# Kernel tuning notes

Hardware: AMD Instinct MI355X
Metric: run time of the kernel (lower is better)

## Reference

```python
import jax, jax.numpy as jnp
import numpy as np
from jax import lax

V, E, Q, D = 100000, 300, 64, 4096
K = 5
NEG_SLOPE = 0.01


def setup_inputs() -> dict:
    key = jax.random.key(0)
    ks = jax.random.split(key, 16)
    return {
        "question": jax.random.randint(ks[0], (Q,), 0, V),
        "doc1": jax.random.randint(ks[1], (D,), 0, V),
        "doc2": jax.random.randint(ks[2], (D,), 0, V),
        "doc1_sim": jax.random.uniform(ks[3], (D, Q), dtype=jnp.float32),
        "doc2_sim": jax.random.uniform(ks[4], (D, Q), dtype=jnp.float32),
        "gaf": jax.random.normal(ks[5], (4,), dtype=jnp.float32),
        "baf": jax.random.normal(ks[6], (4,), dtype=jnp.float32),
        "emb": jax.random.normal(ks[7], (V, E), dtype=jnp.float32) * 0.1,
        "idf": jax.random.uniform(ks[8], (V, 1), dtype=jnp.float32) * 10.0,
        "conv_w": jax.random.normal(ks[9], (E, E, 3), dtype=jnp.float32) * (1.0 / np.sqrt(3 * E)),
        "conv_b": jax.random.normal(ks[10], (E,), dtype=jnp.float32) * 0.01,
        "qw_w": jax.random.normal(ks[11], (1, E + 1), dtype=jnp.float32) * (1.0 / np.sqrt(E + 1)),
        "qw_b": jax.random.normal(ks[12], (1,), dtype=jnp.float32) * 0.01,
        "lin1_w": jax.random.normal(ks[13], (8, 6), dtype=jnp.float32) * (1.0 / np.sqrt(6)),
        "lin2_w": jax.random.normal(ks[14], (1, 8), dtype=jnp.float32) * (1.0 / np.sqrt(8)),
        "out_w": jax.random.normal(ks[15], (1, 5), dtype=jnp.float32) * (1.0 / np.sqrt(5)),
    }


def _leaky(x):
    return jnp.where(x >= 0, x, NEG_SLOPE * x)


def _conv_residual(x, w, b):
    # x: [L, E]. Torch Conv1d(E,E,3,padding=2) followed by slice [1:L+1] is a
    # centered SAME conv; activation applied before the residual add.
    y = lax.conv_general_dilated(x.T[None], w, (1,), [(1, 1)],
                                 dimension_numbers=("NCW", "OIW", "NCW"))
    y = y[0] + b[:, None]            # [E, L]
    return _leaky(y).T + x           # [L, E]


def _cosine(A, B):
    # A: [Q, E], B: [L, E] -> [Q, L]
    num = A @ B.T
    den = jnp.linalg.norm(A, axis=-1)[:, None] * jnp.linalg.norm(B, axis=-1)[None, :]
    return num / den


def _kmax_pool(sim):
    # sim: [Q, L] -> [Q, 2] = (max, mean of top-K)
    top = lax.top_k(sim, K)[0]       # descending [Q, K]
    return jnp.stack([top[:, 0], jnp.mean(top, axis=-1)], axis=-1)


def _get_output(pooled_list, q_weights, lin1_w, lin2_w):
    temp = jnp.concatenate(pooled_list, axis=-1)     # [Q, 6]
    lo = _leaky(temp @ lin1_w.T) @ lin2_w.T          # [Q, 1]
    lo = lo[:, 0] * q_weights
    return jnp.sum(lo) / lo.shape[0]


def reference(question, doc1, doc2, doc1_sim, doc2_sim, gaf, baf,
              emb, idf, conv_w, conv_b, qw_w, qw_b, lin1_w, lin2_w, out_w):
    q_emb = emb[question]            # [Q, E]
    d1_emb = emb[doc1]               # [D, E]
    d2_emb = emb[doc2]

    sim_ins_d1 = _cosine(q_emb, d1_emb)
    sim_ins_d2 = _cosine(q_emb, d2_emb)

    q_conv = _conv_residual(q_emb, conv_w, conv_b)
    d1_conv = _conv_residual(d1_emb, conv_w, conv_b)
    d2_conv = _conv_residual(d2_emb, conv_w, conv_b)

    sim_sen_d1 = _cosine(q_conv, d1_conv)
    sim_sen_d2 = _cosine(q_conv, d2_conv)

    sim_oh_d1 = doc1_sim.T           # [Q, D]
    sim_oh_d2 = doc2_sim.T

    p_oh_d1, p_ins_d1, p_sen_d1 = _kmax_pool(sim_oh_d1), _kmax_pool(sim_ins_d1), _kmax_pool(sim_sen_d1)
    p_oh_d2, p_ins_d2, p_sen_d2 = _kmax_pool(sim_oh_d2), _kmax_pool(sim_ins_d2), _kmax_pool(sim_sen_d2)

    q_idfs = idf[question]           # [Q, 1]
    qw = jnp.concatenate([q_conv, q_idfs], axis=-1) @ qw_w.T + qw_b  # [Q, 1]
    q_weights = jax.nn.softmax(qw[:, 0], axis=-1)

    doc1_emit = _get_output([p_oh_d1, p_ins_d1, p_sen_d1], q_weights, lin1_w, lin2_w)
    doc2_emit = _get_output([p_oh_d2, p_ins_d2, p_sen_d2], q_weights, lin1_w, lin2_w)

    good_feats = jnp.concatenate([gaf, doc1_emit[None]])  # [5]
    bad_feats = jnp.concatenate([baf, doc2_emit[None]])
    good_out = out_w @ good_feats                          # [1]
    bad_out = out_w @ bad_feats

    loss1 = jnp.mean(jnp.maximum(0.0, -(good_out - bad_out) + 1.0))
    return (loss1, good_out, bad_out, loss1, loss1)
```

## Files before the change

### kernel.cpp

```cpp
#include <hip/hip_runtime.h>
#include <math.h>

#define EE 300
#define KP 320
#define LDSW 328
#define QQ 64
#define DD 4096
#define NEG 0.01f

typedef __attribute__((ext_vector_type(8))) short short8;
typedef __attribute__((ext_vector_type(4))) float f32x4;
typedef unsigned short ushort_t;

__device__ inline ushort_t f2bf(float f) {
  unsigned u = __builtin_bit_cast(unsigned, f);
  u += 0x7fff + ((u >> 16) & 1);
  return (ushort_t)(u >> 16);
}
__device__ inline float bf2f(ushort_t h) {
  return __builtin_bit_cast(float, (unsigned)h << 16);
}
__device__ inline void top5_insert(float* t, float v) {
  if (v > t[4]) {
    t[4] = v;
    #pragma unroll
    for (int j = 4; j > 0; --j)
      if (t[j] > t[j - 1]) { float tmp = t[j]; t[j] = t[j - 1]; t[j - 1] = tmp; }
  }
}

#define GATHER_ROWS (66 + 4098 + 4098)
#define GATHER_BLOCKS ((GATHER_ROWS + 3) / 4)
#define WT_BLOCKS 143
#define ZERO_BLOCKS 9
#define OHPOOL_BLOCKS 256
#define PREP_BLOCKS (GATHER_BLOCKS + WT_BLOCKS + ZERO_BLOCKS + OHPOOL_BLOCKS)

__global__ __launch_bounds__(256) void prep(
    const float* __restrict__ emb, const int* __restrict__ question,
    const int* __restrict__ doc1, const int* __restrict__ doc2,
    const float* __restrict__ conv_w,
    const float* __restrict__ doc1_sim, const float* __restrict__ doc2_sim,
    ushort_t* __restrict__ qbe, ushort_t* __restrict__ d1be, ushort_t* __restrict__ d2be,
    ushort_t* __restrict__ qbc, ushort_t* __restrict__ d1bc, ushort_t* __restrict__ d2bc,
    ushort_t* __restrict__ wt2,
    float* __restrict__ nq2, float* __restrict__ nd12, float* __restrict__ nd22,
    float* __restrict__ zero_base, float* __restrict__ pt5) {
  __shared__ float strip[64][33];
  int b = blockIdx.x;
  int tid = threadIdx.x;
  int wv = tid >> 6, lane = tid & 63;
  if (b < GATHER_BLOCKS) {
    int g = b * 4 + wv;
    if (g >= GATHER_ROWS) return;
    int t, row;
    if (g < 66)             { t = 0; row = g; }
    else if (g < 66 + 4098) { t = 1; row = g - 66; }
    else                    { t = 2; row = g - 4164; }
    const int* idx = t == 0 ? question : (t == 1 ? doc1 : doc2);
    int L = t == 0 ? QQ : DD;
    ushort_t* be = t == 0 ? qbe : (t == 1 ? d1be : d2be);
    ushort_t* bc = t == 0 ? qbc : (t == 1 ? d1bc : d2bc);
    float* nrm2 = t == 0 ? nq2 : (t == 1 ? nd12 : nd22);
    if (row == 0 || row == L + 1) {
      for (int i = lane; i < KP; i += 64) be[(size_t)row * KP + i] = 0;
      return;
    }
    int r = row - 1;
    const float* src = emb + (size_t)idx[r] * EE;
    float ss = 0.f;
    for (int i = lane; i < EE; i += 64) {
      float v = src[i];
      be[(size_t)row * KP + i] = f2bf(v);
      ss += v * v;
    }
    for (int i = EE + lane; i < KP; i += 64) {
      be[(size_t)row * KP + i] = 0;
      bc[(size_t)r * KP + i] = 0;
    }
    #pragma unroll
    for (int o = 32; o; o >>= 1) ss += __shfl_xor(ss, o);
    if (lane == 0) nrm2[r] = ss;
  } else if (b < GATHER_BLOCKS + WT_BLOCKS) {
    int f = (b - GATHER_BLOCKS) * 4 + wv;
    if (f >= 570) return;
    int ks = f % 10, n = (f / 10) % 19, tap = f / 190;
    int o = n * 16 + (lane & 15);
    int kbase = ks * 32 + (lane >> 4) * 8;
    ushort_t* dst = wt2 + (size_t)f * 512 + lane * 8;
    #pragma unroll
    for (int e = 0; e < 8; ++e) {
      int k = kbase + e;
      float v = (o < EE && k < EE) ? conv_w[((size_t)o * EE + k) * 3 + tap] : 0.f;
      dst[e] = f2bf(v);
    }
  } else if (b < GATHER_BLOCKS + WT_BLOCKS + ZERO_BLOCKS) {
    int i0 = (b - (GATHER_BLOCKS + WT_BLOCKS)) * 1024 + tid;
    #pragma unroll
    for (int j = 0; j < 4; ++j) {
      int i = i0 + j * 256;
      if (i < 8320) zero_base[i] = 0.f;
    }
  } else {
    int ob = b - (GATHER_BLOCKS + WT_BLOCKS + ZERO_BLOCKS);
    int o = ob >> 7, chunk = ob & 127;
    int ps = o ? 3 : 0;
    const float* dsim = o ? doc2_sim : doc1_sim;
    int l0 = chunk * 32;
    int r = tid >> 3, q0 = (tid & 7) * 8;
    const float* srcp = dsim + (size_t)(l0 + r) * QQ + q0;
    f32x4 v0 = *(const f32x4*)srcp;
    f32x4 v1 = *(const f32x4*)(srcp + 4);
    #pragma unroll
    for (int e = 0; e < 4; ++e) strip[q0 + e][r] = v0[e];
    #pragma unroll
    for (int e = 0; e < 4; ++e) strip[q0 + 4 + e][r] = v1[e];
    __syncthreads();
    if (tid < 64) {
      float t5[5] = {-1e30f, -1e30f, -1e30f, -1e30f, -1e30f};
      #pragma unroll
      for (int l = 0; l < 32; ++l) top5_insert(t5, strip[tid][l]);
      float* dst = pt5 + (((size_t)ps * QQ + tid) * 128 + chunk) * 8;
      *(f32x4*)dst = (f32x4){t5[0], t5[1], t5[2], t5[3]};
      *(f32x4*)(dst + 4) = (f32x4){t5[4], -1e30f, -1e30f, -1e30f};
    }
  }
}

__global__ __launch_bounds__(256) void conv_mfma(
    const ushort_t* __restrict__ wt2, const float* __restrict__ bias,
    const float* __restrict__ qw_w,
    const ushort_t* __restrict__ qbe, const ushort_t* __restrict__ d1be,
    const ushort_t* __restrict__ d2be,
    ushort_t* __restrict__ qbc, ushort_t* __restrict__ d1bc,
    ushort_t* __restrict__ d2bc,
    float* __restrict__ nqc2, float* __restrict__ nd1c2, float* __restrict__ nd2c2,
    float* __restrict__ qwacc) {
  __shared__ ushort_t lds[34 * LDSW];
  int bx = blockIdx.x;
  int t, m0, yh;
  if (bx < 4) { t = 0; m0 = (bx >> 1) * 32; yh = bx & 1; }
  else {
    int i = bx - 4;
    t = 1 + (i >> 8);
    int j = i & 255;
    m0 = (j >> 1) * 32; yh = j & 1;
  }
  const ushort_t* be = t == 0 ? qbe : (t == 1 ? d1be : d2be);
  ushort_t* bc = t == 0 ? qbc : (t == 1 ? d1bc : d2bc);
  float* nc2 = t == 0 ? nqc2 : (t == 1 ? nd1c2 : nd2c2);
  int tid = threadIdx.x;
  for (int s = tid; s < 34 * 40; s += 256) {
    int row = s / 40, col = s - row * 40;
    *(short8*)(&lds[row * LDSW + col * 8]) =
        *(const short8*)(be + (size_t)(m0 + row) * KP + col * 8);
  }
  __syncthreads();
  int wv = tid >> 6, lane = tid & 63, mrow = lane & 15, g = lane >> 4;
  int nstart, ncnt;
  if (yh == 0) { nstart = (wv < 2) ? 3 * wv : 2 * wv + 2; ncnt = (wv < 2) ? 3 : 2; }
  else         { nstart = (wv == 0) ? 10 : 2 * wv + 11;   ncnt = (wv == 0) ? 3 : 2; }
  f32x4 acc[3][2];
  #pragma unroll
  for (int j = 0; j < 3; ++j)
    #pragma unroll
    for (int h = 0; h < 2; ++h) acc[j][h] = (f32x4){0.f, 0.f, 0.f, 0.f};

  for (int tap = 0; tap < 3; ++tap) {
    const ushort_t* alo = &lds[(mrow + tap) * LDSW + g * 8];
    #pragma unroll
    for (int ks = 0; ks < 10; ++ks) {
      short8 a0 = *(const short8*)(alo + ks * 32);
      short8 a1 = *(const short8*)(alo + 16 * LDSW + ks * 32);
      #pragma unroll
      for (int j = 0; j < 3; ++j) {
        if (j < ncnt) {
          short8 bfr = *(const short8*)(wt2 +
              (size_t)((tap * 19 + nstart + j) * 10 + ks) * 512 + lane * 8);
          acc[j][0] = __builtin_amdgcn_mfma_f32_16x16x32_bf16(a0, bfr, acc[j][0], 0, 0, 0);
          acc[j][1] = __builtin_amdgcn_mfma_f32_16x16x32_bf16(a1, bfr, acc[j][1], 0, 0, 0);
        }
      }
    }
  }
  float ss[2][4] = {{0.f,0.f,0.f,0.f},{0.f,0.f,0.f,0.f}};
  float yq[2][4] = {{0.f,0.f,0.f,0.f},{0.f,0.f,0.f,0.f}};
  #pragma unroll
  for (int j = 0; j < 3; ++j) {
    if (j < ncnt) {
      int col = (nstart + j) * 16 + mrow;
      if (col < EE) {
        float bcol = bias[col];
        float qwc = (t == 0) ? qw_w[col] : 0.f;
        #pragma unroll
        for (int h = 0; h < 2; ++h) {
          #pragma unroll
          for (int r = 0; r < 4; ++r) {
            int lrow = h * 16 + g * 4 + r;
            float y = acc[j][h][r] + bcol;
            y = (y >= 0.f) ? y : NEG * y;
            y += bf2f(lds[(1 + lrow) * LDSW + col]);
            bc[(size_t)(m0 + lrow) * KP + col] = f2bf(y);
            ss[h][r] += y * y;
            if (t == 0) yq[h][r] += y * qwc;
          }
        }
      }
    }
  }
  #pragma unroll
  for (int h = 0; h < 2; ++h) {
    #pragma unroll
    for (int r = 0; r < 4; ++r) {
      float s = ss[h][r];
      s += __shfl_xor(s, 1); s += __shfl_xor(s, 2);
      s += __shfl_xor(s, 4); s += __shfl_xor(s, 8);
      if (mrow == 0) atomicAdd(&nc2[m0 + h * 16 + g * 4 + r], s);
      if (t == 0) {
        float sq = yq[h][r];
        sq += __shfl_xor(sq, 1); sq += __shfl_xor(sq, 2);
        sq += __shfl_xor(sq, 4); sq += __shfl_xor(sq, 8);
        if (mrow == 0) atomicAdd(&qwacc[m0 + h * 16 + g * 4 + r], sq);
      }
    }
  }
}

__global__ __launch_bounds__(256) void sim_pool(
    const ushort_t* __restrict__ qbe, const ushort_t* __restrict__ d1be,
    const ushort_t* __restrict__ d2be,
    const ushort_t* __restrict__ qbc, const ushort_t* __restrict__ d1bc,
    const ushort_t* __restrict__ d2bc,
    const float* __restrict__ nq2, const float* __restrict__ nd12,
    const float* __restrict__ nd22, const float* __restrict__ nqc2,
    const float* __restrict__ nd1c2, const float* __restrict__ nd2c2,
    float* __restrict__ pt5) {
  __shared__ ushort_t ldsB[32 * LDSW];
  __shared__ float strip[64][33];
  int s = blockIdx.x >> 7, chunk = blockIdx.x & 127;
  int ps = (s == 0) ? 1 : (s == 1) ? 4 : (s == 2) ? 2 : 5;
  int l0 = chunk * 32;
  const ushort_t* A = (s < 2) ? qbe + KP : qbc;
  const ushort_t* B = s == 0 ? d1be + KP : s == 1 ? d2be + KP
                    : s == 2 ? d1bc : d2bc;
  const float* na2 = (s < 2) ? nq2 : nqc2;
  const float* nb2 = s == 0 ? nd12 : s == 1 ? nd22 : s == 2 ? nd1c2 : nd2c2;
  int tid = threadIdx.x;
  for (int i = tid; i < 32 * 40; i += 256) {
    int row = i / 40, col = i - row * 40;
    *(short8*)(&ldsB[row * LDSW + col * 8]) =
        *(const short8*)(B + (size_t)(l0 + row) * KP + col * 8);
  }
  __syncthreads();
  int wv = tid >> 6, lane = tid & 63, mrow = lane & 15, g = lane >> 4;
  f32x4 acc[2];
  acc[0] = (f32x4){0.f, 0.f, 0.f, 0.f};
  acc[1] = (f32x4){0.f, 0.f, 0.f, 0.f};
  const ushort_t* arow = A + (size_t)(wv * 16 + mrow) * KP + g * 8;
  #pragma unroll
  for (int ks = 0; ks < 10; ++ks) {
    short8 a = *(const short8*)(arow + ks * 32);
    #pragma unroll
    for (int n = 0; n < 2; ++n) {
      short8 bfr = *(const short8*)(&ldsB[(n * 16 + mrow) * LDSW + g * 8 + ks * 32]);
      acc[n] = __builtin_amdgcn_mfma_f32_16x16x32_bf16(a, bfr, acc[n], 0, 0, 0);
    }
  }
  #pragma unroll
  for (int n = 0; n < 2; ++n) {
    int l = n * 16 + mrow;
    float inb = rsqrtf(nb2[l0 + l]);
    #pragma unroll
    for (int r = 0; r < 4; ++r) {
      int q = wv * 16 + g * 4 + r;
      strip[q][l] = acc[n][r] * rsqrtf(na2[q]) * inb;
    }
  }
  __syncthreads();
  if (tid < 64) {
    float t5[5] = {-1e30f, -1e30f, -1e30f, -1e30f, -1e30f};
    #pragma unroll
    for (int l = 0; l < 32; ++l) top5_insert(t5, strip[tid][l]);
    float* dst = pt5 + (((size_t)ps * QQ + tid) * 128 + chunk) * 8;
    *(f32x4*)dst = (f32x4){t5[0], t5[1], t5[2], t5[3]};
    *(f32x4*)(dst + 4) = (f32x4){t5[4], -1e30f, -1e30f, -1e30f};
  }
}

__global__ __launch_bounds__(256) void merge(
    const float* __restrict__ pt5, float* __restrict__ pool) {
  int widx = blockIdx.x * 4 + (threadIdx.x >> 6);
  int lane = threadIdx.x & 63;
  int src = widx >> 6, q = widx & 63;
  const float* p0 = pt5 + (((size_t)src * QQ + q) * 128 + 2 * lane) * 8;
  float t5[5] = {-1e30f, -1e30f, -1e30f, -1e30f, -1e30f};
  #pragma unroll
  for (int c = 0; c < 2; ++c)
    #pragma unroll
    for (int j = 0; j < 5; ++j) top5_insert(t5, p0[c * 8 + j]);
  #pragma unroll
  for (int mask = 1; mask < 64; mask <<= 1) {
    float a[5], bb[5];
    #pragma unroll
    for (int j = 0; j < 5; ++j) { a[j] = t5[j]; bb[j] = __shfl_xor(t5[j], mask); }
    int ia = 0, ib = 0;
    #pragma unroll
    for (int j = 0; j < 5; ++j) t5[j] = (a[ia] >= bb[ib]) ? a[ia++] : bb[ib++];
  }
  if (lane == 0) {
    float sm = t5[0] + t5[1] + t5[2] + t5[3] + t5[4];
    pool[((size_t)src * QQ + q) * 2 + 0] = t5[0];
    pool[((size_t)src * QQ + q) * 2 + 1] = sm * 0.2f;
  }
}

__global__ void final_kernel(
    const float* __restrict__ qwacc, const float* __restrict__ idf,
    const int* __restrict__ question, const float* __restrict__ qw_w,
    const float* __restrict__ qw_b, const float* __restrict__ pool,
    const float* __restrict__ lin1_w, const float* __restrict__ lin2_w,
    const float* __restrict__ out_w, const float* __restrict__ gaf,
    const float* __restrict__ baf, float* __restrict__ out5) {
  int q = threadIdx.x;
  float s = qwacc[q] + qw_b[0] + idf[question[q]] * qw_w[EE];
  float m = s;
  #pragma unroll
  for (int o = 32; o; o >>= 1) m = fmaxf(m, __shfl_xor(m, o));
  float e = expf(s - m);
  float se = e;
  #pragma unroll
  for (int o = 32; o; o >>= 1) se += __shfl_xor(se, o);
  float qwgt = e / se;

  float emit[2];
  for (int doc = 0; doc < 2; ++doc) {
    float temp[6];
    #pragma unroll
    for (int j = 0; j < 3; ++j) {
      temp[2 * j]     = pool[(((size_t)doc * 3 + j) * QQ + q) * 2 + 0];
      temp[2 * j + 1] = pool[(((size_t)doc * 3 + j) * QQ + q) * 2 + 1];
    }
    float lo = 0.f;
    #pragma unroll
    for (int r = 0; r < 8; ++r) {
      float h = 0.f;
      #pragma unroll
      for (int c = 0; c < 6; ++c) h += lin1_w[r * 6 + c] * temp[c];
      h = (h >= 0.f) ? h : NEG * h;
      lo += lin2_w[r] * h;
    }
    lo *= qwgt;
    #pragma unroll
    for (int o = 32; o; o >>= 1) lo += __shfl_xor(lo, o);
    emit[doc] = lo / (float)QQ;
  }
  if (q == 0) {
    float good = out_w[0] * gaf[0] + out_w[1] * gaf[1] + out_w[2] * gaf[2] +
                 out_w[3] * gaf[3] + out_w[4] * emit[0];
    float bad  = out_w[0] * baf[0] + out_w[1] * baf[1] + out_w[2] * baf[2] +
                 out_w[3] * baf[3] + out_w[4] * emit[1];
    float l1 = fmaxf(0.f, -(good - bad) + 1.f);
    out5[0] = l1; out5[1] = good; out5[2] = bad; out5[3] = l1; out5[4] = l1;
  }
}

extern "C" void kernel_launch(void* const* d_in, const int* in_sizes, int n_in,
                              void* d_out, int out_size, void* d_ws, size_t ws_size,
                              hipStream_t stream) {
  (void)in_sizes; (void)n_in; (void)out_size; (void)ws_size;
  const int* question   = (const int*)d_in[0];
  const int* doc1       = (const int*)d_in[1];
  const int* doc2       = (const int*)d_in[2];
  const float* doc1_sim = (const float*)d_in[3];
  const float* doc2_sim = (const float*)d_in[4];
  const float* gaf      = (const float*)d_in[5];
  const float* baf      = (const float*)d_in[6];
  const float* emb      = (const float*)d_in[7];
  const float* idf      = (const float*)d_in[8];
  const float* conv_w   = (const float*)d_in[9];
  const float* conv_b   = (const float*)d_in[10];
  const float* qw_w     = (const float*)d_in[11];
  const float* qw_b     = (const float*)d_in[12];
  const float* lin1_w   = (const float*)d_in[13];
  const float* lin2_w   = (const float*)d_in[14];
  const float* out_w    = (const float*)d_in[15];
  float* out = (float*)d_out;

  char* p = (char*)d_ws;
  ushort_t* qbe  = (ushort_t*)p; p += (size_t)(QQ + 2) * KP * 2;
  ushort_t* d1be = (ushort_t*)p; p += (size_t)(DD + 2) * KP * 2;
  ushort_t* d2be = (ushort_t*)p; p += (size_t)(DD + 2) * KP * 2;
  ushort_t* qbc  = (ushort_t*)p; p += (size_t)QQ * KP * 2;
  ushort_t* d1bc = (ushort_t*)p; p += (size_t)DD * KP * 2;
  ushort_t* d2bc = (ushort_t*)p; p += (size_t)DD * KP * 2;
  ushort_t* wt2  = (ushort_t*)p; p += (size_t)570 * 512 * 2;
  float* nq2   = (float*)p; p += QQ * 4;
  float* nd12  = (float*)p; p += DD * 4;
  float* nd22  = (float*)p; p += DD * 4;
  float* nqc2  = (float*)p; p += QQ * 4;
  float* nd1c2 = (float*)p; p += DD * 4;
  float* nd2c2 = (float*)p; p += DD * 4;
  float* qwacc = (float*)p; p += QQ * 4;
  float* pt5   = (float*)p; p += (size_t)6 * QQ * 128 * 8 * 4;
  float* pool  = (float*)p; p += 6 * QQ * 2 * 4;

  prep<<<PREP_BLOCKS, 256, 0, stream>>>(
      emb, question, doc1, doc2, conv_w, doc1_sim, doc2_sim,
      qbe, d1be, d2be, qbc, d1bc, d2bc, wt2,
      nq2, nd12, nd22, nqc2, pt5);

  conv_mfma<<<516, 256, 0, stream>>>(
      wt2, conv_b, qw_w, qbe, d1be, d2be, qbc, d1bc, d2bc,
      nqc2, nd1c2, nd2c2, qwacc);

  sim_pool<<<512, 256, 0, stream>>>(
      qbe, d1be, d2be, qbc, d1bc, d2bc,
      nq2, nd12, nd22, nqc2, nd1c2, nd2c2, pt5);

  merge<<<96, 256, 0, stream>>>(pt5, pool);

  final_kernel<<<1, 64, 0, stream>>>(qwacc, idf, question, qw_w, qw_b, pool,
                                     lin1_w, lin2_w, out_w, gaf, baf, out);
}
```

Before: 57.59 us.

## Fuse ins-sim into conv kernel, merge pooling into sen-sim and final kernels

The embedding-similarity top-k work now runs as extra blocks inside the conv kernel, since it only depends on the gathered embeddings. The sentence-similarity blocks run alongside the merge of the already-finished pools, and the remaining merges move into the final kernel. Chunks grow from 32 to 64 rows, and the conv tile grows from 32 to 64 rows per block. This removes two launches and halves the partial top-5 buffer. In exchange there are fewer, heavier blocks, more accumulator registers in the conv, and a serial merge loop in a single-block final kernel.

Measured after the change: 129.4 us. +124.8%, slower.

```diff
diff --git a/kernel.cpp b/kernel.cpp
--- a/kernel.cpp
+++ b/kernel.cpp
@@ -28,12 +28,74 @@
       if (t[j] > t[j - 1]) { float tmp = t[j]; t[j] = t[j - 1]; t[j - 1] = tmp; }
   }
 }
+__device__ inline void wave_merge5(float* t5) {
+  #pragma unroll
+  for (int mask = 1; mask < 64; mask <<= 1) {
+    float a[5], bb[5];
+    #pragma unroll
+    for (int j = 0; j < 5; ++j) { a[j] = t5[j]; bb[j] = __shfl_xor(t5[j], mask); }
+    int ia = 0, ib = 0;
+    #pragma unroll
+    for (int j = 0; j < 5; ++j) t5[j] = (a[ia] >= bb[ib]) ? a[ia++] : bb[ib++];
+  }
+}
+
+#define SMEM_BYTES (66 * LDSW * 2)
+
+__device__ void sim64(const ushort_t* __restrict__ A, const ushort_t* __restrict__ B,
+                      const float* __restrict__ na2, const float* __restrict__ nb2,
+                      int chunk, int ps, float* __restrict__ pt5, char* smem) {
+  ushort_t* ldsB = (ushort_t*)smem;
+  float (*strip)[65] = (float(*)[65])smem;
+  int l0 = chunk * 64;
+  int tid = threadIdx.x;
+  for (int i = tid; i < 64 * 40; i += 256) {
+    int row = i / 40, col = i - row * 40;
+    *(short8*)(&ldsB[row * LDSW + col * 8]) =
+        *(const short8*)(B + (size_t)(l0 + row) * KP + col * 8);
+  }
+  __syncthreads();
+  int wv = tid >> 6, lane = tid & 63, mrow = lane & 15, g = lane >> 4;
+  f32x4 acc[4];
+  #pragma unroll
+  for (int n = 0; n < 4; ++n) acc[n] = (f32x4){0.f, 0.f, 0.f, 0.f};
+  const ushort_t* arow = A + (size_t)(wv * 16 + mrow) * KP + g * 8;
+  #pragma unroll
+  for (int ks = 0; ks < 10; ++ks) {
+    short8 a = *(const short8*)(arow + ks * 32);
+    #pragma unroll
+    for (int n = 0; n < 4; ++n) {
+      short8 bfr = *(const short8*)(&ldsB[(n * 16 + mrow) * LDSW + g * 8 + ks * 32]);
+      acc[n] = __builtin_amdgcn_mfma_f32_16x16x32_bf16(a, bfr, acc[n], 0, 0, 0);
+    }
+  }
+  __syncthreads();
+  #pragma unroll
+  for (int n = 0; n < 4; ++n) {
+    int l = n * 16 + mrow;
+    float inb = rsqrtf(nb2[l0 + l]);
+    #pragma unroll
+    for (int r = 0; r < 4; ++r) {
+      int q = wv * 16 + g * 4 + r;
+      strip[q][l] = acc[n][r] * rsqrtf(na2[q]) * inb;
+    }
+  }
+  __syncthreads();
+  if (tid < 64) {
+    float t5[5] = {-1e30f, -1e30f, -1e30f, -1e30f, -1e30f};
+    #pragma unroll
+    for (int l = 0; l < 64; ++l) top5_insert(t5, strip[tid][l]);
+    float* dst = pt5 + (((size_t)ps * QQ + tid) * 64 + chunk) * 8;
+    *(f32x4*)dst = (f32x4){t5[0], t5[1], t5[2], t5[3]};
+    *(f32x4*)(dst + 4) = (f32x4){t5[4], -1e30f, -1e30f, -1e30f};
+  }
+}
 
 #define GATHER_ROWS (66 + 4098 + 4098)
 #define GATHER_BLOCKS ((GATHER_ROWS + 3) / 4)
 #define WT_BLOCKS 143
 #define ZERO_BLOCKS 9
-#define OHPOOL_BLOCKS 256
+#define OHPOOL_BLOCKS 128
 #define PREP_BLOCKS (GATHER_BLOCKS + WT_BLOCKS + ZERO_BLOCKS + OHPOOL_BLOCKS)
 
 __global__ __launch_bounds__(256) void prep(
@@ -46,7 +108,7 @@
     ushort_t* __restrict__ wt2,
     float* __restrict__ nq2, float* __restrict__ nd12, float* __restrict__ nd22,
     float* __restrict__ zero_base, float* __restrict__ pt5) {
-  __shared__ float strip[64][33];
+  __shared__ float strip[64][65];
   int b = blockIdx.x;
   int tid = threadIdx.x;
   int wv = tid >> 6, lane = tid & 63;
@@ -103,54 +165,64 @@
     }
   } else {
     int ob = b - (GATHER_BLOCKS + WT_BLOCKS + ZERO_BLOCKS);
-    int o = ob >> 7, chunk = ob & 127;
+    int o = ob >> 6, chunk = ob & 63;
     int ps = o ? 3 : 0;
     const float* dsim = o ? doc2_sim : doc1_sim;
-    int l0 = chunk * 32;
-    int r = tid >> 3, q0 = (tid & 7) * 8;
+    int l0 = chunk * 64;
+    int r = tid >> 2, q0 = (tid & 3) * 16;
     const float* srcp = dsim + (size_t)(l0 + r) * QQ + q0;
-    f32x4 v0 = *(const f32x4*)srcp;
-    f32x4 v1 = *(const f32x4*)(srcp + 4);
-    #pragma unroll
-    for (int e = 0; e < 4; ++e) strip[q0 + e][r] = v0[e];
-    #pragma unroll
-    for (int e = 0; e < 4; ++e) strip[q0 + 4 + e][r] = v1[e];
+    #pragma unroll
+    for (int c = 0; c < 4; ++c) {
+      f32x4 v = *(const f32x4*)(srcp + c * 4);
+      #pragma unroll
+      for (int e = 0; e < 4; ++e) strip[q0 + c * 4 + e][r] = v[e];
+    }
     __syncthreads();
     if (tid < 64) {
       float t5[5] = {-1e30f, -1e30f, -1e30f, -1e30f, -1e30f};
       #pragma unroll
-      for (int l = 0; l < 32; ++l) top5_insert(t5, strip[tid][l]);
-      float* dst = pt5 + (((size_t)ps * QQ + tid) * 128 + chunk) * 8;
+      for (int l = 0; l < 64; ++l) top5_insert(t5, strip[tid][l]);
+      float* dst = pt5 + (((size_t)ps * QQ + tid) * 64 + chunk) * 8;
       *(f32x4*)dst = (f32x4){t5[0], t5[1], t5[2], t5[3]};
       *(f32x4*)(dst + 4) = (f32x4){t5[4], -1e30f, -1e30f, -1e30f};
     }
   }
 }
 
-__global__ __launch_bounds__(256) void conv_mfma(
+__global__ __launch_bounds__(256) void conv_insim(
     const ushort_t* __restrict__ wt2, const float* __restrict__ bias,
     const float* __restrict__ qw_w,
     const ushort_t* __restrict__ qbe, const ushort_t* __restrict__ d1be,
     const ushort_t* __restrict__ d2be,
     ushort_t* __restrict__ qbc, ushort_t* __restrict__ d1bc,
     ushort_t* __restrict__ d2bc,
+    const float* __restrict__ nq2, const float* __restrict__ nd12,
+    const float* __restrict__ nd22,
     float* __restrict__ nqc2, float* __restrict__ nd1c2, float* __restrict__ nd2c2,
-    float* __restrict__ qwacc) {
-  __shared__ ushort_t lds[34 * LDSW];
+    float* __restrict__ qwacc, float* __restrict__ pt5) {
+  __shared__ __align__(16) char smem[SMEM_BYTES];
   int bx = blockIdx.x;
+  int tid = threadIdx.x;
+  if (bx >= 258) {
+    int task = bx - 258;
+    int s = task >> 6, chunk = task & 63;
+    sim64(qbe + KP, s == 0 ? d1be + KP : d2be + KP,
+          nq2, s == 0 ? nd12 : nd22, chunk, s == 0 ? 1 : 4, pt5, smem);
+    return;
+  }
+  ushort_t* lds = (ushort_t*)smem;
   int t, m0, yh;
-  if (bx < 4) { t = 0; m0 = (bx >> 1) * 32; yh = bx & 1; }
+  if (bx < 2) { t = 0; m0 = 0; yh = bx; }
   else {
-    int i = bx - 4;
-    t = 1 + (i >> 8);
-    int j = i & 255;
-    m0 = (j >> 1) * 32; yh = j & 1;
+    int i = bx - 2;
+    t = 1 + (i >> 7);
+    int j = i & 127;
+    m0 = (j >> 1) * 64; yh = j & 1;
   }
   const ushort_t* be = t == 0 ? qbe : (t == 1 ? d1be : d2be);
   ushort_t* bc = t == 0 ? qbc : (t == 1 ? d1bc : d2bc);
   float* nc2 = t == 0 ? nqc2 : (t == 1 ? nd1c2 : nd2c2);
-  int tid = threadIdx.x;
-  for (int s = tid; s < 34 * 40; s += 256) {
+  for (int s = tid; s < 66 * 40; s += 256) {
     int row = s / 40, col = s - row * 40;
     *(short8*)(&lds[row * LDSW + col * 8]) =
         *(const short8*)(be + (size_t)(m0 + row) * KP + col * 8);
@@ -160,31 +232,34 @@
   int nstart, ncnt;
   if (yh == 0) { nstart = (wv < 2) ? 3 * wv : 2 * wv + 2; ncnt = (wv < 2) ? 3 : 2; }
   else         { nstart = (wv == 0) ? 10 : 2 * wv + 11;   ncnt = (wv == 0) ? 3 : 2; }
-  f32x4 acc[3][2];
+  f32x4 acc[3][4];
   #pragma unroll
   for (int j = 0; j < 3; ++j)
     #pragma unroll
-    for (int h = 0; h < 2; ++h) acc[j][h] = (f32x4){0.f, 0.f, 0.f, 0.f};
+    for (int h = 0; h < 4; ++h) acc[j][h] = (f32x4){0.f, 0.f, 0.f, 0.f};
 
   for (int tap = 0; tap < 3; ++tap) {
     const ushort_t* alo = &lds[(mrow + tap) * LDSW + g * 8];
     #pragma unroll
     for (int ks = 0; ks < 10; ++ks) {
-      short8 a0 = *(const short8*)(alo + ks * 32);
-      short8 a1 = *(const short8*)(alo + 16 * LDSW + ks * 32);
+      short8 a[4];
+      #pragma unroll
+      for (int h = 0; h < 4; ++h)
+        a[h] = *(const short8*)(alo + h * 16 * LDSW + ks * 32);
       #pragma unroll
       for (int j = 0; j < 3; ++j) {
         if (j < ncnt) {
           short8 bfr = *(const short8*)(wt2 +
               (size_t)((tap * 19 + nstart + j) * 10 + ks) * 512 + lane * 8);
-          acc[j][0] = __builtin_amdgcn_mfma_f32_16x16x32_bf16(a0, bfr, acc[j][0], 0, 0, 0);
-          acc[j][1] = __builtin_amdgcn_mfma_f32_16x16x32_bf16(a1, bfr, acc[j][1], 0, 0, 0);
+          #pragma unroll
+          for (int h = 0; h < 4; ++h)
+            acc[j][h] = __builtin_amdgcn_mfma_f32_16x16x32_bf16(a[h], bfr, acc[j][h], 0, 0, 0);
         }
       }
     }
   }
-  float ss[2][4] = {{0.f,0.f,0.f,0.f},{0.f,0.f,0.f,0.f}};
-  float yq[2][4] = {{0.f,0.f,0.f,0.f},{0.f,0.f,0.f,0.f}};
+  float ss[4][4] = {{0.f},{0.f},{0.f},{0.f}};
+  float yq[4][4] = {{0.f},{0.f},{0.f},{0.f}};
   #pragma unroll
   for (int j = 0; j < 3; ++j) {
     if (j < ncnt) {
@@ -193,7 +268,7 @@
         float bcol = bias[col];
         float qwc = (t == 0) ? qw_w[col] : 0.f;
         #pragma unroll
-        for (int h = 0; h < 2; ++h) {
+        for (int h = 0; h < 4; ++h) {
           #pragma unroll
           for (int r = 0; r < 4; ++r) {
             int lrow = h * 16 + g * 4 + r;
@@ -209,7 +284,7 @@
     }
   }
   #pragma unroll
-  for (int h = 0; h < 2; ++h) {
+  for (int h = 0; h < 4; ++h) {
     #pragma unroll
     for (int r = 0; r < 4; ++r) {
       float s = ss[h][r];
@@ -226,141 +301,108 @@
   }
 }
 
-__global__ __launch_bounds__(256) void sim_pool(
-    const ushort_t* __restrict__ qbe, const ushort_t* __restrict__ d1be,
-    const ushort_t* __restrict__ d2be,
+__global__ __launch_bounds__(256) void sensim_merge(
     const ushort_t* __restrict__ qbc, const ushort_t* __restrict__ d1bc,
     const ushort_t* __restrict__ d2bc,
-    const float* __restrict__ nq2, const float* __restrict__ nd12,
-    const float* __restrict__ nd22, const float* __restrict__ nqc2,
-    const float* __restrict__ nd1c2, const float* __restrict__ nd2c2,
-    float* __restrict__ pt5) {
-  __shared__ ushort_t ldsB[32 * LDSW];
-  __shared__ float strip[64][33];
-  int s = blockIdx.x >> 7, chunk = blockIdx.x & 127;
-  int ps = (s == 0) ? 1 : (s == 1) ? 4 : (s == 2) ? 2 : 5;
-  int l0 = chunk * 32;
-  const ushort_t* A = (s < 2) ? qbe + KP : qbc;
-  const ushort_t* B = s == 0 ? d1be + KP : s == 1 ? d2be + KP
-                    : s == 2 ? d1bc : d2bc;
-  const float* na2 = (s < 2) ? nq2 : nqc2;
-  const float* nb2 = s == 0 ? nd12 : s == 1 ? nd22 : s == 2 ? nd1c2 : nd2c2;
+    const float* __restrict__ nqc2, const float* __restrict__ nd1c2,
+    const float* __restrict__ nd2c2,
+    float* __restrict__ pt5, float* __restrict__ pool) {
+  __shared__ __align__(16) char smem[SMEM_BYTES];
+  int bx = blockIdx.x;
   int tid = threadIdx.x;
-  for (int i = tid; i < 32 * 40; i += 256) {
-    int row = i / 40, col = i - row * 40;
-    *(short8*)(&ldsB[row * LDSW + col * 8]) =
-        *(const short8*)(B + (size_t)(l0 + row) * KP + col * 8);
-  }
-  __syncthreads();
-  int wv = tid >> 6, lane = tid & 63, mrow = lane & 15, g = lane >> 4;
-  f32x4 acc[2];
-  acc[0] = (f32x4){0.f, 0.f, 0.f, 0.f};
-  acc[1] = (f32x4){0.f, 0.f, 0.f, 0.f};
-  const ushort_t* arow = A + (size_t)(wv * 16 + mrow) * KP + g * 8;
-  #pragma unroll
-  for (int ks = 0; ks < 10; ++ks) {
-    short8 a = *(const short8*)(arow + ks * 32);
-    #pragma unroll
-    for (int n = 0; n < 2; ++n) {
-      short8 bfr = *(const short8*)(&ldsB[(n * 16 + mrow) * LDSW + g * 8 + ks * 32]);
-      acc[n] = __builtin_amdgcn_mfma_f32_16x16x32_bf16(a, bfr, acc[n], 0, 0, 0);
-    }
-  }
-  #pragma unroll
-  for (int n = 0; n < 2; ++n) {
-    int l = n * 16 + mrow;
-    float inb = rsqrtf(nb2[l0 + l]);
-    #pragma unroll
-    for (int r = 0; r < 4; ++r) {
-      int q = wv * 16 + g * 4 + r;
-      strip[q][l] = acc[n][r] * rsqrtf(na2[q]) * inb;
+  if (bx < 128) {
+    int s = bx >> 6, chunk = bx & 63;
+    sim64(qbc, s == 0 ? d1bc : d2bc,
+          nqc2, s == 0 ? nd1c2 : nd2c2, chunk, s == 0 ? 2 : 5, pt5, smem);
+    return;
+  }
+  int wv = tid >> 6, lane = tid & 63;
+  int widx = (bx - 128) * 4 + wv;
+  int s4 = widx >> 6, q = widx & 63;
+  int ps = (s4 == 0) ? 0 : (s4 == 1) ? 1 : (s4 == 2) ? 3 : 4;
+  const float* p0 = pt5 + (((size_t)ps * QQ + q) * 64 + lane) * 8;
+  float t5[5];
+  #pragma unroll
+  for (int j = 0; j < 5; ++j) t5[j] = p0[j];
+  wave_merge5(t5);
+  if (lane == 0) {
+    float sm = t5[0] + t5[1] + t5[2] + t5[3] + t5[4];
+    pool[((size_t)ps * QQ + q) * 2 + 0] = t5[0];
+    pool[((size_t)ps * QQ + q) * 2 + 1] = sm * 0.2f;
+  }
+}
+
+__global__ __launch_bounds__(256) void final_kernel(
+    const float* __restrict__ pt5, const float* __restrict__ pool,
+    const float* __restrict__ qwacc, const float* __restrict__ idf,
+    const int* __restrict__ question, const float* __restrict__ qw_w,
+    const float* __restrict__ qw_b, const float* __restrict__ lin1_w,
+    const float* __restrict__ lin2_w, const float* __restrict__ out_w,
+    const float* __restrict__ gaf, const float* __restrict__ baf,
+    float* __restrict__ out5) {
+  __shared__ float poolL[6][QQ][2];
+  int tid = threadIdx.x, wv = tid >> 6, lane = tid & 63;
+  for (int i = tid; i < 6 * QQ * 2; i += 256) {
+    int ps = i / (QQ * 2);
+    if (ps != 2 && ps != 5) (&poolL[0][0][0])[i] = pool[i];
+  }
+  for (int it = 0; it < 32; ++it) {
+    int pairIdx = wv * 32 + it;
+    int ps = (pairIdx < 64) ? 2 : 5;
+    int q = pairIdx & 63;
+    const float* p0 = pt5 + (((size_t)ps * QQ + q) * 64 + lane) * 8;
+    float t5[5];
+    #pragma unroll
+    for (int j = 0; j < 5; ++j) t5[j] = p0[j];
+    wave_merge5(t5);
+    if (lane == 0) {
+      float sm = t5[0] + t5[1] + t5[2] + t5[3] + t5[4];
+      poolL[ps][q][0] = t5[0];
+      poolL[ps][q][1] = sm * 0.2f;
     }
   }
   __syncthreads();
   if (tid < 64) {
-    float t5[5] = {-1e30f, -1e30f, -1e30f, -1e30f, -1e30f};
-    #pragma unroll
-    for (int l = 0; l < 32; ++l) top5_insert(t5, strip[tid][l]);
-    float* dst = pt5 + (((size_t)ps * QQ + tid) * 128 + chunk) * 8;
-    *(f32x4*)dst = (f32x4){t5[0], t5[1], t5[2], t5[3]};
-    *(f32x4*)(dst + 4) = (f32x4){t5[4], -1e30f, -1e30f, -1e30f};
-  }
-}
-
-__global__ __launch_bounds__(256) void merge(
-    const float* __restrict__ pt5, float* __restrict__ pool) {
-  int widx = blockIdx.x * 4 + (threadIdx.x >> 6);
-  int lane = threadIdx.x & 63;
-  int src = widx >> 6, q = widx & 63;
-  const float* p0 = pt5 + (((size_t)src * QQ + q) * 128 + 2 * lane) * 8;
-  float t5[5] = {-1e30f, -1e30f, -1e30f, -1e30f, -1e30f};
-  #pragma unroll
-  for (int c = 0; c < 2; ++c)
-    #pragma unroll
-    for (int j = 0; j < 5; ++j) top5_insert(t5, p0[c * 8 + j]);
-  #pragma unroll
-  for (int mask = 1; mask < 64; mask <<= 1) {
-    float a[5], bb[5];
-    #pragma unroll
-    for (int j = 0; j < 5; ++j) { a[j] = t5[j]; bb[j] = __shfl_xor(t5[j], mask); }
-    int ia = 0, ib = 0;
-    #pragma unroll
-    for (int j = 0; j < 5; ++j) t5[j] = (a[ia] >= bb[ib]) ? a[ia++] : bb[ib++];
-  }
-  if (lane == 0) {
-    float sm = t5[0] + t5[1] + t5[2] + t5[3] + t5[4];
-    pool[((size_t)src * QQ + q) * 2 + 0] = t5[0];
-    pool[((size_t)src * QQ + q) * 2 + 1] = sm * 0.2f;
-  }
-}
-
-__global__ void final_kernel(
-    const float* __restrict__ qwacc, const float* __restrict__ idf,
-    const int* __restrict__ question, const float* __restrict__ qw_w,
-    const float* __restrict__ qw_b, const float* __restrict__ pool,
-    const float* __restrict__ lin1_w, const float* __restrict__ lin2_w,
-    const float* __restrict__ out_w, const float* __restrict__ gaf,
-    const float* __restrict__ baf, float* __restrict__ out5) {
-  int q = threadIdx.x;
-  float s = qwacc[q] + qw_b[0] + idf[question[q]] * qw_w[EE];
-  float m = s;
-  #pragma unroll
-  for (int o = 32; o; o >>= 1) m = fmaxf(m, __shfl_xor(m, o));
-  float e = expf(s - m);
-  float se = e;
-  #pragma unroll
-  for (int o = 32; o; o >>= 1) se += __shfl_xor(se, o);
-  float qwgt = e / se;
-
-  float emit[2];
-  for (int doc = 0; doc < 2; ++doc) {
-    float temp[6];
-    #pragma unroll
-    for (int j = 0; j < 3; ++j) {
-      temp[2 * j]     = pool[(((size_t)doc * 3 + j) * QQ + q) * 2 + 0];
-      temp[2 * j + 1] = pool[(((size_t)doc * 3 + j) * QQ + q) * 2 + 1];
-    }
-    float lo = 0.f;
-    #pragma unroll
-    for (int r = 0; r < 8; ++r) {
-      float h = 0.f;
-      #pragma unroll
-      for (int c = 0; c < 6; ++c) h += lin1_w[r * 6 + c] * temp[c];
-      h = (h >= 0.f) ? h : NEG * h;
-      lo += lin2_w[r] * h;
-    }
-    lo *= qwgt;
-    #pragma unroll
-    for (int o = 32; o; o >>= 1) lo += __shfl_xor(lo, o);
-    emit[doc] = lo / (float)QQ;
-  }
-  if (q == 0) {
-    float good = out_w[0] * gaf[0] + out_w[1] * gaf[1] + out_w[2] * gaf[2] +
-                 out_w[3] * gaf[3] + out_w[4] * emit[0];
-    float bad  = out_w[0] * baf[0] + out_w[1] * baf[1] + out_w[2] * baf[2] +
-                 out_w[3] * baf[3] + out_w[4] * emit[1];
-    float l1 = fmaxf(0.f, -(good - bad) + 1.f);
-    out5[0] = l1; out5[1] = good; out5[2] = bad; out5[3] = l1; out5[4] = l1;
+    int q = tid;
+    float s = qwacc[q] + qw_b[0] + idf[question[q]] * qw_w[EE];
+    float m = s;
+    #pragma unroll
+    for (int o = 32; o; o >>= 1) m = fmaxf(m, __shfl_xor(m, o));
+    float e = expf(s - m);
+    float se = e;
+    #pragma unroll
+    for (int o = 32; o; o >>= 1) se += __shfl_xor(se, o);
+    float qwgt = e / se;
+    float emit[2];
+    for (int doc = 0; doc < 2; ++doc) {
+      float temp[6];
+      #pragma unroll
+      for (int j = 0; j < 3; ++j) {
+        temp[2 * j]     = poolL[doc * 3 + j][q][0];
+        temp[2 * j + 1] = poolL[doc * 3 + j][q][1];
+      }
+      float lo = 0.f;
+      #pragma unroll
+      for (int r = 0; r < 8; ++r) {
+        float h = 0.f;
+        #pragma unroll
+        for (int c = 0; c < 6; ++c) h += lin1_w[r * 6 + c] * temp[c];
+        h = (h >= 0.f) ? h : NEG * h;
+        lo += lin2_w[r] * h;
+      }
+      lo *= qwgt;
+      #pragma unroll
+      for (int o = 32; o; o >>= 1) lo += __shfl_xor(lo, o);
+      emit[doc] = lo / (float)QQ;
+    }
+    if (q == 0) {
+      float good = out_w[0] * gaf[0] + out_w[1] * gaf[1] + out_w[2] * gaf[2] +
+                   out_w[3] * gaf[3] + out_w[4] * emit[0];
+      float bad  = out_w[0] * baf[0] + out_w[1] * baf[1] + out_w[2] * baf[2] +
+                   out_w[3] * baf[3] + out_w[4] * emit[1];
+      float l1 = fmaxf(0.f, -(good - bad) + 1.f);
+      out5[0] = l1; out5[1] = good; out5[2] = bad; out5[3] = l1; out5[4] = l1;
+    }
   }
 }
 
@@ -401,7 +443,7 @@
   float* nd1c2 = (float*)p; p += DD * 4;
   float* nd2c2 = (float*)p; p += DD * 4;
   float* qwacc = (float*)p; p += QQ * 4;
-  float* pt5   = (float*)p; p += (size_t)6 * QQ * 128 * 8 * 4;
+  float* pt5   = (float*)p; p += (size_t)6 * QQ * 64 * 8 * 4;
   float* pool  = (float*)p; p += 6 * QQ * 2 * 4;
 
   prep<<<PREP_BLOCKS, 256, 0, stream>>>(
@@ -409,16 +451,14 @@
       qbe, d1be, d2be, qbc, d1bc, d2bc, wt2,
       nq2, nd12, nd22, nqc2, pt5);
 
-  conv_mfma<<<516, 256, 0, stream>>>(
+  conv_insim<<<386, 256, 0, stream>>>(
       wt2, conv_b, qw_w, qbe, d1be, d2be, qbc, d1bc, d2bc,
-      nqc2, nd1c2, nd2c2, qwacc);
-
-  sim_pool<<<512, 256, 0, stream>>>(
-      qbe, d1be, d2be, qbc, d1bc, d2bc,
-      nq2, nd12, nd22, nqc2, nd1c2, nd2c2, pt5);
-
-  merge<<<96, 256, 0, stream>>>(pt5, pool);
-
-  final_kernel<<<1, 64, 0, stream>>>(qwacc, idf, question, qw_w, qw_b, pool,
-                                     lin1_w, lin2_w, out_w, gaf, baf, out);
-}
+      nq2, nd12, nd22, nqc2, nd1c2, nd2c2, qwacc, pt5);
+
+  sensim_merge<<<192, 256, 0, stream>>>(
+      qbc, d1bc, d2bc, nqc2, nd1c2, nd2c2, pt5, pool);
+
+  final_kernel<<<1, 256, 0, stream>>>(
+      pt5, pool, qwacc, idf, question, qw_w, qw_b,
+      lin1_w, lin2_w, out_w, gaf, baf, out);
+}
```
